# Kernel tuning notes

Measured on AMD Instinct MI355X. Metric: run time of the kernel, lower is better.

The kernel has to match this reference:

```python
import jax, jax.numpy as jnp
import numpy as np

N_NODES = 100000
N_EDGES = 800000
IN_DIM = 128
HID_DIM = 128
OUT_DIM = 128


def setup_inputs() -> dict:
    key = jax.random.key(0)
    ks = jax.random.split(key, 10)
    feat1 = jax.random.normal(ks[0], (N_NODES, IN_DIM), dtype=jnp.float32)
    feat2 = jax.random.normal(ks[1], (N_NODES, IN_DIM), dtype=jnp.float32)
    # GraphConv weights (Glorot-ish scale) and biases
    W1 = jax.random.normal(ks[2], (IN_DIM, HID_DIM), dtype=jnp.float32) * (1.0 / np.sqrt(IN_DIM))
    b1 = jnp.zeros((HID_DIM,), dtype=jnp.float32)
    W2 = jax.random.normal(ks[3], (HID_DIM, OUT_DIM), dtype=jnp.float32) * (1.0 / np.sqrt(HID_DIM))
    b2 = jnp.zeros((OUT_DIM,), dtype=jnp.float32)
    src1 = jax.random.randint(ks[4], (N_EDGES,), 0, N_NODES, dtype=jnp.int32)
    dst1 = jax.random.randint(ks[5], (N_EDGES,), 0, N_NODES, dtype=jnp.int32)
    src2 = jax.random.randint(ks[6], (N_EDGES,), 0, N_NODES, dtype=jnp.int32)
    dst2 = jax.random.randint(ks[7], (N_EDGES,), 0, N_NODES, dtype=jnp.int32)
    return {"feat1": feat1, "feat2": feat2, "W1": W1, "b1": b1, "W2": W2, "b2": b2,
            "src1": src1, "dst1": dst1, "src2": src2, "dst2": dst2}


def _graph_conv(x, src, dst, W, b, n_nodes):
    # DGL GraphConv, norm='both': h = D_in^{-1/2} A D_out^{-1/2} x W + b
    ones = jnp.ones(src.shape, dtype=x.dtype)
    deg_out = jax.ops.segment_sum(ones, src, num_segments=n_nodes)
    deg_in = jax.ops.segment_sum(ones, dst, num_segments=n_nodes)
    x = x * (jnp.maximum(deg_out, 1.0) ** -0.5)[:, None]
    x = x @ W                                 # apply linear before aggregation (equivalent math)
    agg = jax.ops.segment_sum(x[src], dst, num_segments=n_nodes)  # SpMM: gather + scatter-add
    return agg * (jnp.maximum(deg_in, 1.0) ** -0.5)[:, None] + b


def _encode(x, src, dst, Ws, bs, n_nodes):
    for i in range(len(Ws) - 1):
        x = jax.nn.relu(_graph_conv(x, src, dst, Ws[i], bs[i], n_nodes))
    return _graph_conv(x, src, dst, Ws[-1], bs[-1], n_nodes)


def reference(feat1, feat2, W1, b1, W2, b2, src1, dst1, src2, dst2):
    n = feat1.shape[0]
    Ws, bs = [W1, W2], [b1, b2]
    h1 = _encode(feat1, src1, dst1, Ws, bs, n)
    h2 = _encode(feat2, src2, dst2, Ws, bs, n)
    # per-feature z-score; torch std(0) is unbiased (ddof=1)
    z1 = (h1 - h1.mean(0)) / h1.std(0, ddof=1)
    z2 = (h2 - h2.mean(0)) / h2.std(0, ddof=1)
    return (z1, z2)
```

## Files before the change

### kernel.cpp

```cpp
#include <hip/hip_runtime.h>
#include <cstdint>
#include <cstddef>


#define SCAN_CHUNK 1024
#define NSLICES 64
#define HWORDS 25000

typedef __attribute__((ext_vector_type(8))) short bf16x8;
typedef __attribute__((ext_vector_type(4))) float f32x4;

__device__ __forceinline__ unsigned short f2bf(float f) {
    unsigned int u = __float_as_uint(f);
    unsigned int r = (u + 0x7FFFu + ((u >> 16) & 1u)) >> 16;
    return (unsigned short)r;
}
__device__ __forceinline__ float bflo(unsigned int u) { return __uint_as_float(u << 16); }
__device__ __forceinline__ float bfhi(unsigned int u) { return __uint_as_float(u & 0xffff0000u); }

__global__ __launch_bounds__(1024) void hist_kernel(
    const int* __restrict__ src1, const int* __restrict__ dst1,
    const int* __restrict__ src2, const int* __restrict__ dst2,
    unsigned int* __restrict__ part, int E)
{
    __shared__ unsigned int h[HWORDS];
    const int bid = blockIdx.x;
    const int a = bid / NSLICES, s = bid % NSLICES;
    const int* idx = a == 0 ? src1 : a == 1 ? dst1 : a == 2 ? src2 : dst2;

    for (int i = threadIdx.x; i < HWORDS; i += 1024) h[i] = 0u;
    __syncthreads();

    const int lo = (int)((long long)s * E / NSLICES);
    const int hi = (int)((long long)(s + 1) * E / NSLICES);
    for (int i = lo + threadIdx.x; i < hi; i += 1024) {
        unsigned int v = (unsigned int)idx[i];
        atomicAdd(&h[v >> 2], 1u << ((v & 3u) << 3));
    }
    __syncthreads();

    unsigned int* out = part + (size_t)bid * HWORDS;
    for (int i = threadIdx.x; i < HWORDS; i += 1024) out[i] = h[i];
}

__global__ __launch_bounds__(256) void hist_reduce(
    const unsigned int* __restrict__ part, int* __restrict__ deg, int M)
{
    int i = blockIdx.x * blockDim.x + threadIdx.x;
    if (i >= 4 * HWORDS) return;
    int a = i / HWORDS, w = i % HWORDS;
    const unsigned int* p = part + (size_t)a * NSLICES * HWORDS + w;
    unsigned int accA = 0u, accB = 0u;
#pragma unroll
    for (int s = 0; s < NSLICES; ++s) {
        unsigned int v = p[(size_t)s * HWORDS];
        accA += v & 0x00FF00FFu;
        accB += (v >> 8) & 0x00FF00FFu;
    }
    int4 r = make_int4((int)(accA & 0xFFFFu), (int)(accB & 0xFFFFu),
                       (int)(accA >> 16),     (int)(accB >> 16));
    *(int4*)(deg + (size_t)a * M + 4 * w) = r;
}

__global__ void scan_block_sums(const int* __restrict__ deg, int* __restrict__ partials,
                                int M, int goff)
{
    __shared__ int sd[256];
    const int g = blockIdx.y + goff;
    const int* d = deg + (size_t)(2 * g + 1) * M;
    int base = blockIdx.x * SCAN_CHUNK + threadIdx.x * 4;
    int s = 0;
#pragma unroll
    for (int j = 0; j < 4; ++j) { int i = base + j; if (i < M) s += d[i]; }
    sd[threadIdx.x] = s;
    __syncthreads();
    for (int off = 128; off > 0; off >>= 1) {
        if (threadIdx.x < off) sd[threadIdx.x] += sd[threadIdx.x + off];
        __syncthreads();
    }
    if (threadIdx.x == 0) partials[g * 256 + blockIdx.x] = sd[0];
}

__global__ void scan_partials(const int* __restrict__ partials, int* __restrict__ blockoff,
                              int P, int goff)
{
    __shared__ int sd[256];
    const int g = blockIdx.y + goff;
    const int* pp = partials + g * 256;
    int v = threadIdx.x < P ? pp[threadIdx.x] : 0;
    sd[threadIdx.x] = v;
    __syncthreads();
    for (int off = 1; off < 256; off <<= 1) {
        int t = threadIdx.x >= off ? sd[threadIdx.x - off] : 0;
        __syncthreads();
        sd[threadIdx.x] += t;
        __syncthreads();
    }
    if (threadIdx.x < P) blockoff[g * 256 + threadIdx.x] = sd[threadIdx.x] - v;
}

__global__ void scan_write(const int* __restrict__ deg, const int* __restrict__ blockoff,
                           int* rp0, int* rp1, int* cu0, int* cu1, int M, int goff)
{
    __shared__ int sd[256];
    const int g = blockIdx.y + goff;
    const int* d = deg + (size_t)(2 * g + 1) * M;
    int* rowptr = g ? rp1 : rp0;
    int* cursor = g ? cu1 : cu0;
    int base = blockIdx.x * SCAN_CHUNK + threadIdx.x * 4;
    int d0 = 0, d1 = 0, d2 = 0, d3 = 0;
    if (base + 0 < M) d0 = d[base + 0];
    if (base + 1 < M) d1 = d[base + 1];
    if (base + 2 < M) d2 = d[base + 2];
    if (base + 3 < M) d3 = d[base + 3];
    int tot = d0 + d1 + d2 + d3;
    sd[threadIdx.x] = tot;
    __syncthreads();
    for (int off = 1; off < 256; off <<= 1) {
        int t = threadIdx.x >= off ? sd[threadIdx.x - off] : 0;
        __syncthreads();
        sd[threadIdx.x] += t;
        __syncthreads();
    }
    int texcl = sd[threadIdx.x] - tot + blockoff[g * 256 + blockIdx.x];
    int p0 = texcl + d0, p1 = p0 + d1, p2 = p1 + d2, p3 = p2 + d3;
    if (base + 0 < M) { rowptr[base + 1] = p0; cursor[base + 0] = texcl; }
    if (base + 1 < M) { rowptr[base + 2] = p1; cursor[base + 1] = p0; }
    if (base + 2 < M) { rowptr[base + 3] = p2; cursor[base + 2] = p1; }
    if (base + 3 < M) { rowptr[base + 4] = p3; cursor[base + 3] = p2; }
    if (blockIdx.x == 0 && threadIdx.x == 0) rowptr[0] = 0;
}

__global__ __launch_bounds__(256) void csr_fill(
    const int* s0, const int* s1, const int* d0, const int* d1,
    int* cu0, int* cu1, int* co0, int* co1, int E, int M, int goff)
{
    const int g = blockIdx.y + goff;
    const int* src = g ? s1 : s0;
    const int* dst = g ? d1 : d0;
    int* cursor = g ? cu1 : cu0;
    int* colidx = g ? co1 : co0;

    const int grp = blockIdx.x & 7;
    const unsigned int nlo = (unsigned int)((long long)grp * M / 8);
    const unsigned int nspan = (unsigned int)((long long)(grp + 1) * M / 8) - nlo;
    const int nb = gridDim.x >> 3;
    const int bi = blockIdx.x >> 3;
    const int stride = nb * 256;

    for (int e = bi * 256 + threadIdx.x; e < E; e += stride) {
        int d = dst[e];
        int sv = src[e];
        if ((unsigned int)(d - nlo) < nspan) {
            int pos = atomicAdd(&cursor[d], 1);
            colidx[pos] = sv;
        }
    }
}

__global__ void wswz_kernel(const float* __restrict__ Wa, const float* __restrict__ Wb,
                            unsigned short* __restrict__ Wz)
{
    int i = blockIdx.x * 256 + threadIdx.x;
    const float* W = (i < 16384) ? Wa : Wb;
    int ii = i & 16383;
    int j = ii & 7, l = (ii >> 3) & 63, s = (ii >> 9) & 3, t = ii >> 11;
    int k = s * 32 + ((l >> 4) * 8) + j;
    int n = t * 16 + (l & 15);
    Wz[i] = f2bf(W[k * 128 + n]);
}

__global__ __launch_bounds__(256) void mfma_gemm(
    const float* X0, const float* X1, const unsigned short* __restrict__ Wz,
    const int* __restrict__ deg, unsigned short* Y0, unsigned short* Y1,
    int M, int goff)
{
    __shared__ __align__(16) unsigned short Abf[64 * 136];
    const int g = blockIdx.y + goff;
    const float* X = g ? X1 : X0;
    const int* deg_out = deg + (size_t)2 * g * M;
    unsigned short* Yh = g ? Y1 : Y0;
    const int tid  = threadIdx.x;
    const int row0 = blockIdx.x * 64;

#pragma unroll
    for (int i = 0; i < 8; ++i) {
        int idx = tid + i * 256;
        int r = idx >> 5, c4 = idx & 31;
        int gr = row0 + r;
        float4 v = make_float4(0.f, 0.f, 0.f, 0.f);
        if (gr < M) {
            v = ((const float4*)X)[(size_t)gr * 32 + c4];
            float so = rsqrtf(fmaxf((float)deg_out[gr], 1.f));
            v.x *= so; v.y *= so; v.z *= so; v.w *= so;
        }
        unsigned int lo = (unsigned int)f2bf(v.x) | ((unsigned int)f2bf(v.y) << 16);
        unsigned int hi = (unsigned int)f2bf(v.z) | ((unsigned int)f2bf(v.w) << 16);
        *(uint2*)(Abf + r * 136 + c4 * 4) = make_uint2(lo, hi);
    }
    __syncthreads();

    const int w = tid >> 6, lane = tid & 63;
    const int m = lane & 15, quad = lane >> 4;

    bf16x8 a[4];
#pragma unroll
    for (int s = 0; s < 4; ++s)
        a[s] = *(const bf16x8*)(Abf + (w * 16 + m) * 136 + s * 32 + quad * 8);

#pragma unroll
    for (int t = 0; t < 8; ++t) {
        f32x4 acc = {0.f, 0.f, 0.f, 0.f};
#pragma unroll
        for (int s = 0; s < 4; ++s) {
            bf16x8 b = *(const bf16x8*)(Wz + (((t * 4 + s) * 64 + lane) << 3));
            acc = __builtin_amdgcn_mfma_f32_16x16x32_bf16(a[s], b, acc, 0, 0, 0);
        }
        int gr  = row0 + w * 16 + quad * 4;
        int col = t * 16 + m;
#pragma unroll
        for (int r = 0; r < 4; ++r) {
            if (gr + r < M) Yh[(size_t)(gr + r) * 128 + col] = f2bf(acc[r]);
        }
    }
}

__device__ __forceinline__ void xcd_tile(int nb, int xcdmap, int goff,
                                         int& g, int& tile)
{
    if (xcdmap) {
        int bid = blockIdx.x;
        int grp = bid & 7;
        g = grp >> 2;
        tile = (bid >> 3) * 4 + (grp & 3);
    } else {
        g = goff;
        tile = blockIdx.x;
    }
}

#define G16_ACC(v)                                                              \
    a0 += bflo(v.x); a1 += bfhi(v.x); a2 += bflo(v.y); a3 += bfhi(v.y);         \
    a4 += bflo(v.z); a5 += bfhi(v.z); a6 += bflo(v.w); a7 += bfhi(v.w);

#define GATHER_ROW16                                                            \
    {                                                                           \
        for (; e + 8 <= end; e += 8) {                                          \
            int c0 = colidx[e+0], c1 = colidx[e+1], c2 = colidx[e+2], c3 = colidx[e+3]; \
            int c4_ = colidx[e+4], c5 = colidx[e+5], c6 = colidx[e+6], c7 = colidx[e+7]; \
            uint4 v0 = Yv[(size_t)c0 * 16 + lane16];                            \
            uint4 v1 = Yv[(size_t)c1 * 16 + lane16];                            \
            uint4 v2 = Yv[(size_t)c2 * 16 + lane16];                            \
            uint4 v3 = Yv[(size_t)c3 * 16 + lane16];                            \
            uint4 v4 = Yv[(size_t)c4_ * 16 + lane16];                           \
            uint4 v5 = Yv[(size_t)c5 * 16 + lane16];                            \
            uint4 v6 = Yv[(size_t)c6 * 16 + lane16];                            \
            uint4 v7 = Yv[(size_t)c7 * 16 + lane16];                            \
            G16_ACC(v0) G16_ACC(v1) G16_ACC(v2) G16_ACC(v3)                     \
            G16_ACC(v4) G16_ACC(v5) G16_ACC(v6) G16_ACC(v7)                     \
        }                                                                       \
        if (e + 4 <= end) {                                                     \
            int c0 = colidx[e+0], c1 = colidx[e+1], c2 = colidx[e+2], c3 = colidx[e+3]; \
            uint4 v0 = Yv[(size_t)c0 * 16 + lane16];                            \
            uint4 v1 = Yv[(size_t)c1 * 16 + lane16];                            \
            uint4 v2 = Yv[(size_t)c2 * 16 + lane16];                            \
            uint4 v3 = Yv[(size_t)c3 * 16 + lane16];                            \
            G16_ACC(v0) G16_ACC(v1) G16_ACC(v2) G16_ACC(v3)                     \
            e += 4;                                                             \
        }                                                                       \
        for (; e < end; ++e) {                                                  \
            int c = colidx[e];                                                  \
            uint4 v = Yv[(size_t)c * 16 + lane16];                              \
            G16_ACC(v)                                                          \
        }                                                                       \
    }

__global__ __launch_bounds__(256) void spmm_gemm(
    const uint4* Y0, const uint4* Y1, const int* rp0, const int* rp1,
    const int* ci0, const int* ci1, const unsigned short* __restrict__ Wz,
    const int* __restrict__ deg, const float* __restrict__ bias,
    unsigned short* O0, unsigned short* O1, int M, int nb, int xcdmap, int goff)
{
    __shared__ __align__(16) unsigned short Abf[64 * 136];
    int g, tile;
    xcd_tile(nb, xcdmap, goff, g, tile);
    if (tile >= nb) return;
    const uint4* Yv = g ? Y1 : Y0;
    const int* rowptr = g ? rp1 : rp0;
    const int* colidx = g ? ci1 : ci0;
    const int* deg_out = deg + (size_t)2 * g * M;
    const int* deg_in  = deg_out + M;
    unsigned short* Yh2 = g ? O1 : O0;

    const int tid  = threadIdx.x;
    const int row0 = tile * 64;
    const int lane16 = tid & 15;
    const int ng = tid >> 4;
    const float4 bv0 = ((const float4*)bias)[lane16 * 2];
    const float4 bv1 = ((const float4*)bias)[lane16 * 2 + 1];

#pragma unroll 1
    for (int p = 0; p < 4; ++p) {
        const int r = p * 16 + ng;
        const int node = row0 + r;
        float a0=0.f,a1=0.f,a2=0.f,a3=0.f,a4=0.f,a5=0.f,a6=0.f,a7=0.f;
        if (node < M) {
            int e = rowptr[node], end = rowptr[node + 1];
            GATHER_ROW16
            float si = rsqrtf(fmaxf((float)deg_in[node], 1.f));
            float so = rsqrtf(fmaxf((float)deg_out[node], 1.f));
            a0 = fmaxf(a0 * si + bv0.x, 0.f) * so;
            a1 = fmaxf(a1 * si + bv0.y, 0.f) * so;
            a2 = fmaxf(a2 * si + bv0.z, 0.f) * so;
            a3 = fmaxf(a3 * si + bv0.w, 0.f) * so;
            a4 = fmaxf(a4 * si + bv1.x, 0.f) * so;
            a5 = fmaxf(a5 * si + bv1.y, 0.f) * so;
            a6 = fmaxf(a6 * si + bv1.z, 0.f) * so;
            a7 = fmaxf(a7 * si + bv1.w, 0.f) * so;
        }
        uint4 wv;
        wv.x = (unsigned int)f2bf(a0) | ((unsigned int)f2bf(a1) << 16);
        wv.y = (unsigned int)f2bf(a2) | ((unsigned int)f2bf(a3) << 16);
        wv.z = (unsigned int)f2bf(a4) | ((unsigned int)f2bf(a5) << 16);
        wv.w = (unsigned int)f2bf(a6) | ((unsigned int)f2bf(a7) << 16);
        *(uint4*)(Abf + r * 136 + lane16 * 8) = wv;
    }
    __syncthreads();

    const int w = tid >> 6, lane = tid & 63;
    const int m = lane & 15, quad = lane >> 4;

    bf16x8 a[4];
#pragma unroll
    for (int s = 0; s < 4; ++s)
        a[s] = *(const bf16x8*)(Abf + (w * 16 + m) * 136 + s * 32 + quad * 8);

#pragma unroll
    for (int t = 0; t < 8; ++t) {
        f32x4 acc = {0.f, 0.f, 0.f, 0.f};
#pragma unroll
        for (int s = 0; s < 4; ++s) {
            bf16x8 b = *(const bf16x8*)(Wz + (((t * 4 + s) * 64 + lane) << 3));
            acc = __builtin_amdgcn_mfma_f32_16x16x32_bf16(a[s], b, acc, 0, 0, 0);
        }
        int gr  = row0 + w * 16 + quad * 4;
        int col = t * 16 + m;
#pragma unroll
        for (int r = 0; r < 4; ++r) {
            if (gr + r < M) Yh2[(size_t)(gr + r) * 128 + col] = f2bf(acc[r]);
        }
    }
}

__global__ __launch_bounds__(256) void spmm_stats(
    const uint4* Y0, const uint4* Y1, const int* rp0, const int* rp1,
    const int* ci0, const int* ci1, const int* __restrict__ deg,
    const float* __restrict__ bias, float* __restrict__ Z,
    double* __restrict__ gsum, double* __restrict__ gsumsq,
    int M, int nb, int xcdmap, int goff)
{
    __shared__ float lsum[16][128], lsq[16][128];
    int g, tile;
    xcd_tile(nb, xcdmap, goff, g, tile);
    if (tile >= nb) return;
    const uint4* Yv = g ? Y1 : Y0;
    const int* rowptr = g ? rp1 : rp0;
    const int* colidx = g ? ci1 : ci0;
    const int* deg_in = deg + (size_t)(2 * g + 1) * M;
    float* Zg = Z + (size_t)g * M * 128;
    double* gs = gsum + g * 128;
    double* gq = gsumsq + g * 128;

    const int tid  = threadIdx.x;
    const int row0 = tile * 64;
    const int lane16 = tid & 15;
    const int ng = tid >> 4;
    const float4 bv0 = ((const float4*)bias)[lane16 * 2];
    const float4 bv1 = ((const float4*)bias)[lane16 * 2 + 1];

    float s0=0.f,s1=0.f,s2=0.f,s3=0.f,s4=0.f,s5=0.f,s6=0.f,s7=0.f;
    float q0=0.f,q1=0.f,q2=0.f,q3=0.f,q4=0.f,q5=0.f,q6=0.f,q7=0.f;

#pragma unroll 1
    for (int p = 0; p < 4; ++p) {
        const int node = row0 + p * 16 + ng;
        if (node >= M) continue;
        float a0=0.f,a1=0.f,a2=0.f,a3=0.f,a4=0.f,a5=0.f,a6=0.f,a7=0.f;
        int e = rowptr[node], end = rowptr[node + 1];
        GATHER_ROW16
        float si = rsqrtf(fmaxf((float)deg_in[node], 1.f));
        float h0 = a0 * si + bv0.x, h1 = a1 * si + bv0.y;
        float h2 = a2 * si + bv0.z, h3 = a3 * si + bv0.w;
        float h4 = a4 * si + bv1.x, h5 = a5 * si + bv1.y;
        float h6 = a6 * si + bv1.z, h7 = a7 * si + bv1.w;
        ((float4*)Zg)[(size_t)node * 32 + lane16 * 2]     = make_float4(h0, h1, h2, h3);
        ((float4*)Zg)[(size_t)node * 32 + lane16 * 2 + 1] = make_float4(h4, h5, h6, h7);
        s0 += h0; s1 += h1; s2 += h2; s3 += h3;
        s4 += h4; s5 += h5; s6 += h6; s7 += h7;
        q0 += h0*h0; q1 += h1*h1; q2 += h2*h2; q3 += h3*h3;
        q4 += h4*h4; q5 += h5*h5; q6 += h6*h6; q7 += h7*h7;
    }

    const int cb = lane16 * 8;
    lsum[ng][cb+0]=s0; lsum[ng][cb+1]=s1; lsum[ng][cb+2]=s2; lsum[ng][cb+3]=s3;
    lsum[ng][cb+4]=s4; lsum[ng][cb+5]=s5; lsum[ng][cb+6]=s6; lsum[ng][cb+7]=s7;
    lsq[ng][cb+0]=q0; lsq[ng][cb+1]=q1; lsq[ng][cb+2]=q2; lsq[ng][cb+3]=q3;
    lsq[ng][cb+4]=q4; lsq[ng][cb+5]=q5; lsq[ng][cb+6]=q6; lsq[ng][cb+7]=q7;
    __syncthreads();

    if (tid < 128) {
        float s = 0.f;
#pragma unroll
        for (int g2 = 0; g2 < 16; ++g2) s += lsum[g2][tid];
        atomicAdd(&gs[tid], (double)s);
    } else {
        int c = tid - 128;
        float q = 0.f;
#pragma unroll
        for (int g2 = 0; g2 < 16; ++g2) q += lsq[g2][c];
        atomicAdd(&gq[c], (double)q);
    }
}

__global__ void meanstd_kernel(const double* __restrict__ gsum,
                               const double* __restrict__ gsumsq, int M,
                               float* __restrict__ mean, float* __restrict__ istd)
{
    int c = threadIdx.x;
    double mu  = gsum[c] / (double)M;
    double var = (gsumsq[c] - gsum[c] * mu) / (double)(M - 1);
    mean[c] = (float)mu;
    istd[c] = (float)(1.0 / sqrt(var));
}

__global__ __launch_bounds__(256) void normalize_kernel(
    float* __restrict__ Z, const float* __restrict__ mean,
    const float* __restrict__ istd, int n4_per_g, int n4tot)
{
    int i = blockIdx.x * blockDim.x + threadIdx.x;
    if (i >= n4tot) return;
    int gb = (i >= n4_per_g) ? 128 : 0;
    float4 v = ((float4*)Z)[i];
    int c4 = gb + ((i & 31) << 2);
    v.x = (v.x - mean[c4 + 0]) * istd[c4 + 0];
    v.y = (v.y - mean[c4 + 1]) * istd[c4 + 1];
    v.z = (v.z - mean[c4 + 2]) * istd[c4 + 2];
    v.w = (v.w - mean[c4 + 3]) * istd[c4 + 3];
    ((float4*)Z)[i] = v;
}

extern "C" void kernel_launch(void* const* d_in, const int* in_sizes, int n_in,
                              void* d_out, int out_size, void* d_ws, size_t ws_size,
                              hipStream_t stream)
{
    const float* feat1 = (const float*)d_in[0];
    const float* feat2 = (const float*)d_in[1];
    const float* W1    = (const float*)d_in[2];
    const float* b1    = (const float*)d_in[3];
    const float* W2    = (const float*)d_in[4];
    const float* b2    = (const float*)d_in[5];
    const int*   src1  = (const int*)d_in[6];
    const int*   dst1  = (const int*)d_in[7];
    const int*   src2  = (const int*)d_in[8];
    const int*   dst2  = (const int*)d_in[9];
    float* out = (float*)d_out;

    const int M = in_sizes[0] / 128;
    const int E = in_sizes[6];

    char* p0 = (char*)d_ws;
    char* p = p0;
    auto alloc = [&](size_t b) -> char* {
        char* r = p; p += (b + 255) & ~(size_t)255; return r;
    };

    double* gsum = (double*)alloc(256 * 8);
    double* gsq  = (double*)alloc(256 * 8);
    float*  mean = (float*)alloc(256 * 4);
    float*  istd = (float*)alloc(256 * 4);
    unsigned short* Wz = (unsigned short*)alloc(32768 * 2);
    int* deg = (int*)alloc((size_t)4 * M * 4);
    int* spart = (int*)alloc(512 * 4);
    int* blockoff = (int*)alloc(512 * 4);

    const size_t bytesRP = (size_t)(M + 1) * 4;
    const size_t bytesCU = (size_t)M * 4;
    const size_t bytesCI = (size_t)E * 4;
    const size_t bytesYh = (size_t)M * 128 * 2;
    const size_t bytesHP = (size_t)4 * NSLICES * HWORDS * 4;

    size_t fixed = (size_t)(p - p0);
    size_t need_merged = fixed + 2 * ((bytesRP + 255 & ~(size_t)255) +
                                      (bytesCU + 255 & ~(size_t)255) +
                                      (bytesCI + 255 & ~(size_t)255) +
                                      2 * ((bytesYh + 255 & ~(size_t)255)));
    const bool merged = ws_size >= need_merged + 4096;

    int *rpA, *rpB, *cuA, *cuB, *ciA, *ciB;
    unsigned short *YhA0, *YhA1, *YhB0, *YhB1;
    unsigned int* hpart;

    if (merged) {
        rpA = (int*)alloc(bytesRP);  rpB = (int*)alloc(bytesRP);
        cuA = (int*)alloc(bytesCU);  cuB = (int*)alloc(bytesCU);
        ciA = (int*)alloc(bytesCI);  ciB = (int*)alloc(bytesCI);
        YhA0 = (unsigned short*)alloc(bytesYh);
        YhA1 = (unsigned short*)alloc(bytesYh);
        YhB0 = (unsigned short*)alloc(bytesYh);
        YhB1 = (unsigned short*)alloc(bytesYh);
        hpart = (unsigned int*)YhA0;
    } else {
        rpA = (int*)alloc(bytesRP);  rpB = rpA;
        cuA = (int*)alloc(bytesCU);  cuB = cuA;
        ciA = (int*)alloc(bytesCI);  ciB = ciA;
        YhA0 = (unsigned short*)alloc(bytesYh);  YhA1 = YhA0;
        char* scratch = alloc(bytesHP + bytesYh);
        hpart = (unsigned int*)scratch;
        YhB0 = (unsigned short*)(scratch + bytesHP); YhB1 = YhB0;
    }

    unsigned short* Wz1 = Wz;
    unsigned short* Wz2 = Wz + 16384;

    const int BLK = 256;
    const int gemm_blocks = (M + 63) / 64;
    const int P = (M + SCAN_CHUNK - 1) / SCAN_CHUNK;
    const int NG = merged ? 2 : 1;

    hist_kernel<<<4 * NSLICES, 1024, 0, stream>>>(src1, dst1, src2, dst2, hpart, E);
    hist_reduce<<<(4 * HWORDS + BLK - 1) / BLK, BLK, 0, stream>>>(hpart, deg, M);
    wswz_kernel<<<128, BLK, 0, stream>>>(W1, W2, Wz);

    for (int g0 = 0; g0 < 2; g0 += NG) {
        dim3 gP(P, NG), gF(2048, NG), gG(gemm_blocks, NG);
        int spmm_blocks = merged ? 8 * ((2 * gemm_blocks + 7) / 8) : gemm_blocks;
        int xcdmap = merged ? 1 : 0;

        scan_block_sums<<<gP, BLK, 0, stream>>>(deg, spart, M, g0);
        scan_partials<<<dim3(1, NG), BLK, 0, stream>>>(spart, blockoff, P, g0);
        scan_write<<<gP, BLK, 0, stream>>>(deg, blockoff, rpA, rpB, cuA, cuB, M, g0);
        csr_fill<<<gF, BLK, 0, stream>>>(src1, src2, dst1, dst2, cuA, cuB, ciA, ciB, E, M, g0);

        mfma_gemm<<<gG, BLK, 0, stream>>>(feat1, feat2, Wz1, deg, YhA0, YhA1, M, g0);

        spmm_gemm<<<spmm_blocks, BLK, 0, stream>>>(
            (const uint4*)YhA0, (const uint4*)YhA1, rpA, rpB, ciA, ciB,
            Wz2, deg, b1, YhB0, YhB1, M, gemm_blocks, xcdmap, g0);

        hipMemsetAsync(gsum, 0, 2 * 256 * sizeof(double), stream);
        spmm_stats<<<spmm_blocks, BLK, 0, stream>>>(
            (const uint4*)YhB0, (const uint4*)YhB1, rpA, rpB, ciA, ciB,
            deg, b2, out, gsum, gsq, M, gemm_blocks, xcdmap, g0);

        meanstd_kernel<<<1, NG * 128, 0, stream>>>(
            gsum + g0 * 128, gsq + g0 * 128, M, mean + g0 * 128, istd + g0 * 128);
        int n4g = M * 32, n4tot = NG * n4g;
        normalize_kernel<<<(n4tot + BLK - 1) / BLK, BLK, 0, stream>>>(
            out + (size_t)g0 * M * 128, mean + g0 * 128, istd + g0 * 128, n4g, n4tot);
    }
}
```

Baseline: 531.8 us.

## Bucket SpMM gathers by source-node range and stage column indices in LDS

The SpMM gather in both the GEMM-fused and stats kernels now stages each tile's column indices in shared memory, falling back to global reads if the tile has more than ECAP edges. Edges are then processed in 8 passes, one per source-node range, so that at any moment all blocks touch a smaller slice of the feature table, which should raise L2/MALL hit rates. In exchange, every edge index is read and tested 8 times, the unrolling of the inner loop is lost (one load in flight per row instead of 8), and 32 fp32 accumulators per thread raise register pressure.

```diff
diff --git a/kernel.cpp b/kernel.cpp
--- a/kernel.cpp
+++ b/kernel.cpp
@@ -6,6 +6,8 @@
 #define SCAN_CHUNK 1024
 #define NSLICES 64
 #define HWORDS 25000
+#define NBUCK 8
+#define ECAP 2048
 
 typedef __attribute__((ext_vector_type(8))) short bf16x8;
 typedef __attribute__((ext_vector_type(4))) float f32x4;
@@ -239,39 +241,29 @@
     }
 }
 
-#define G16_ACC(v)                                                              \
-    a0 += bflo(v.x); a1 += bfhi(v.x); a2 += bflo(v.y); a3 += bfhi(v.y);         \
-    a4 += bflo(v.z); a5 += bfhi(v.z); a6 += bflo(v.w); a7 += bfhi(v.w);
-
-#define GATHER_ROW16                                                            \
+#define BUCKET_GATHER(ACC)                                                      \
     {                                                                           \
-        for (; e + 8 <= end; e += 8) {                                          \
-            int c0 = colidx[e+0], c1 = colidx[e+1], c2 = colidx[e+2], c3 = colidx[e+3]; \
-            int c4_ = colidx[e+4], c5 = colidx[e+5], c6 = colidx[e+6], c7 = colidx[e+7]; \
-            uint4 v0 = Yv[(size_t)c0 * 16 + lane16];                            \
-            uint4 v1 = Yv[(size_t)c1 * 16 + lane16];                            \
-            uint4 v2 = Yv[(size_t)c2 * 16 + lane16];                            \
-            uint4 v3 = Yv[(size_t)c3 * 16 + lane16];                            \
-            uint4 v4 = Yv[(size_t)c4_ * 16 + lane16];                           \
-            uint4 v5 = Yv[(size_t)c5 * 16 + lane16];                            \
-            uint4 v6 = Yv[(size_t)c6 * 16 + lane16];                            \
-            uint4 v7 = Yv[(size_t)c7 * 16 + lane16];                            \
-            G16_ACC(v0) G16_ACC(v1) G16_ACC(v2) G16_ACC(v3)                     \
-            G16_ACC(v4) G16_ACC(v5) G16_ACC(v6) G16_ACC(v7)                     \
-        }                                                                       \
-        if (e + 4 <= end) {                                                     \
-            int c0 = colidx[e+0], c1 = colidx[e+1], c2 = colidx[e+2], c3 = colidx[e+3]; \
-            uint4 v0 = Yv[(size_t)c0 * 16 + lane16];                            \
-            uint4 v1 = Yv[(size_t)c1 * 16 + lane16];                            \
-            uint4 v2 = Yv[(size_t)c2 * 16 + lane16];                            \
-            uint4 v3 = Yv[(size_t)c3 * 16 + lane16];                            \
-            G16_ACC(v0) G16_ACC(v1) G16_ACC(v2) G16_ACC(v3)                     \
-            e += 4;                                                             \
-        }                                                                       \
-        for (; e < end; ++e) {                                                  \
-            int c = colidx[e];                                                  \
-            uint4 v = Yv[(size_t)c * 16 + lane16];                              \
-            G16_ACC(v)                                                          \
+        for (int b = 0; b < NBUCK; ++b) {                                       \
+            const unsigned int blo = (unsigned int)((long long)b * M / NBUCK);  \
+            const unsigned int bspan =                                          \
+                (unsigned int)((long long)(b + 1) * M / NBUCK) - blo;           \
+            _Pragma("unroll")                                                   \
+            for (int p = 0; p < 4; ++p) {                                       \
+                const int rr = p * 16 + ng;                                     \
+                if (row0 + rr >= M) continue;                                   \
+                int e  = lrp[rr] - base0;                                       \
+                int e1 = lrp[rr + 1] - base0;                                   \
+                for (; e < e1; ++e) {                                           \
+                    int c = ovf ? colidx[base0 + e] : els[e];                   \
+                    if ((unsigned int)(c - blo) < bspan) {                      \
+                        uint4 v = Yv[(size_t)c * 16 + lane16];                  \
+                        ACC[p][0] += bflo(v.x); ACC[p][1] += bfhi(v.x);         \
+                        ACC[p][2] += bflo(v.y); ACC[p][3] += bfhi(v.y);         \
+                        ACC[p][4] += bflo(v.z); ACC[p][5] += bfhi(v.z);         \
+                        ACC[p][6] += bflo(v.w); ACC[p][7] += bfhi(v.w);         \
+                    }                                                           \
+                }                                                               \
+            }                                                                   \
         }                                                                       \
     }
 
@@ -282,6 +274,8 @@
     unsigned short* O0, unsigned short* O1, int M, int nb, int xcdmap, int goff)
 {
     __shared__ __align__(16) unsigned short Abf[64 * 136];
+    __shared__ int els[ECAP];
+    __shared__ int lrp[68];
     int g, tile;
     xcd_tile(nb, xcdmap, goff, g, tile);
     if (tile >= nb) return;
@@ -296,34 +290,50 @@
     const int row0 = tile * 64;
     const int lane16 = tid & 15;
     const int ng = tid >> 4;
+
+    const int nrow = (M - row0 < 64) ? (M - row0) : 64;
+    if (tid <= nrow) lrp[tid] = rowptr[row0 + tid];
+    __syncthreads();
+    const int base0 = lrp[0];
+    const int len = lrp[nrow] - base0;
+    const bool ovf = len > ECAP;
+    if (!ovf) for (int i = tid; i < len; i += 256) els[i] = colidx[base0 + i];
+    __syncthreads();
+
+    float acc[4][8];
+#pragma unroll
+    for (int p = 0; p < 4; ++p)
+#pragma unroll
+        for (int j = 0; j < 8; ++j) acc[p][j] = 0.f;
+
+    BUCKET_GATHER(acc)
+
     const float4 bv0 = ((const float4*)bias)[lane16 * 2];
     const float4 bv1 = ((const float4*)bias)[lane16 * 2 + 1];
-
-#pragma unroll 1
+#pragma unroll
     for (int p = 0; p < 4; ++p) {
-        const int r = p * 16 + ng;
-        const int node = row0 + r;
-        float a0=0.f,a1=0.f,a2=0.f,a3=0.f,a4=0.f,a5=0.f,a6=0.f,a7=0.f;
+        const int rr = p * 16 + ng;
+        const int node = row0 + rr;
+        float a0 = 0.f, a1 = 0.f, a2 = 0.f, a3 = 0.f;
+        float a4 = 0.f, a5 = 0.f, a6 = 0.f, a7 = 0.f;
         if (node < M) {
-            int e = rowptr[node], end = rowptr[node + 1];
-            GATHER_ROW16
             float si = rsqrtf(fmaxf((float)deg_in[node], 1.f));
             float so = rsqrtf(fmaxf((float)deg_out[node], 1.f));
-            a0 = fmaxf(a0 * si + bv0.x, 0.f) * so;
-            a1 = fmaxf(a1 * si + bv0.y, 0.f) * so;
-            a2 = fmaxf(a2 * si + bv0.z, 0.f) * so;
-            a3 = fmaxf(a3 * si + bv0.w, 0.f) * so;
-            a4 = fmaxf(a4 * si + bv1.x, 0.f) * so;
-            a5 = fmaxf(a5 * si + bv1.y, 0.f) * so;
-            a6 = fmaxf(a6 * si + bv1.z, 0.f) * so;
-            a7 = fmaxf(a7 * si + bv1.w, 0.f) * so;
+            a0 = fmaxf(acc[p][0] * si + bv0.x, 0.f) * so;
+            a1 = fmaxf(acc[p][1] * si + bv0.y, 0.f) * so;
+            a2 = fmaxf(acc[p][2] * si + bv0.z, 0.f) * so;
+            a3 = fmaxf(acc[p][3] * si + bv0.w, 0.f) * so;
+            a4 = fmaxf(acc[p][4] * si + bv1.x, 0.f) * so;
+            a5 = fmaxf(acc[p][5] * si + bv1.y, 0.f) * so;
+            a6 = fmaxf(acc[p][6] * si + bv1.z, 0.f) * so;
+            a7 = fmaxf(acc[p][7] * si + bv1.w, 0.f) * so;
         }
         uint4 wv;
         wv.x = (unsigned int)f2bf(a0) | ((unsigned int)f2bf(a1) << 16);
         wv.y = (unsigned int)f2bf(a2) | ((unsigned int)f2bf(a3) << 16);
         wv.z = (unsigned int)f2bf(a4) | ((unsigned int)f2bf(a5) << 16);
         wv.w = (unsigned int)f2bf(a6) | ((unsigned int)f2bf(a7) << 16);
-        *(uint4*)(Abf + r * 136 + lane16 * 8) = wv;
+        *(uint4*)(Abf + rr * 136 + lane16 * 8) = wv;
     }
     __syncthreads();
 
@@ -337,17 +347,17 @@
 
 #pragma unroll
     for (int t = 0; t < 8; ++t) {
-        f32x4 acc = {0.f, 0.f, 0.f, 0.f};
+        f32x4 acc2 = {0.f, 0.f, 0.f, 0.f};
 #pragma unroll
         for (int s = 0; s < 4; ++s) {
             bf16x8 b = *(const bf16x8*)(Wz + (((t * 4 + s) * 64 + lane) << 3));
-            acc = __builtin_amdgcn_mfma_f32_16x16x32_bf16(a[s], b, acc, 0, 0, 0);
+            acc2 = __builtin_amdgcn_mfma_f32_16x16x32_bf16(a[s], b, acc2, 0, 0, 0);
         }
         int gr  = row0 + w * 16 + quad * 4;
         int col = t * 16 + m;
 #pragma unroll
         for (int r = 0; r < 4; ++r) {
-            if (gr + r < M) Yh2[(size_t)(gr + r) * 128 + col] = f2bf(acc[r]);
+            if (gr + r < M) Yh2[(size_t)(gr + r) * 128 + col] = f2bf(acc2[r]);
         }
     }
 }
@@ -360,6 +370,8 @@
     int M, int nb, int xcdmap, int goff)
 {
     __shared__ float lsum[16][128], lsq[16][128];
+    __shared__ int els[ECAP];
+    __shared__ int lrp[68];
     int g, tile;
     xcd_tile(nb, xcdmap, goff, g, tile);
     if (tile >= nb) return;
@@ -375,24 +387,38 @@
     const int row0 = tile * 64;
     const int lane16 = tid & 15;
     const int ng = tid >> 4;
+
+    const int nrow = (M - row0 < 64) ? (M - row0) : 64;
+    if (tid <= nrow) lrp[tid] = rowptr[row0 + tid];
+    __syncthreads();
+    const int base0 = lrp[0];
+    const int len = lrp[nrow] - base0;
+    const bool ovf = len > ECAP;
+    if (!ovf) for (int i = tid; i < len; i += 256) els[i] = colidx[base0 + i];
+    __syncthreads();
+
+    float acc[4][8];
+#pragma unroll
+    for (int p = 0; p < 4; ++p)
+#pragma unroll
+        for (int j = 0; j < 8; ++j) acc[p][j] = 0.f;
+
+    BUCKET_GATHER(acc)
+
     const float4 bv0 = ((const float4*)bias)[lane16 * 2];
     const float4 bv1 = ((const float4*)bias)[lane16 * 2 + 1];
-
     float s0=0.f,s1=0.f,s2=0.f,s3=0.f,s4=0.f,s5=0.f,s6=0.f,s7=0.f;
     float q0=0.f,q1=0.f,q2=0.f,q3=0.f,q4=0.f,q5=0.f,q6=0.f,q7=0.f;
 
-#pragma unroll 1
+#pragma unroll
     for (int p = 0; p < 4; ++p) {
         const int node = row0 + p * 16 + ng;
         if (node >= M) continue;
-        float a0=0.f,a1=0.f,a2=0.f,a3=0.f,a4=0.f,a5=0.f,a6=0.f,a7=0.f;
-        int e = rowptr[node], end = rowptr[node + 1];
-        GATHER_ROW16
         float si = rsqrtf(fmaxf((float)deg_in[node], 1.f));
-        float h0 = a0 * si + bv0.x, h1 = a1 * si + bv0.y;
-        float h2 = a2 * si + bv0.z, h3 = a3 * si + bv0.w;
-        float h4 = a4 * si + bv1.x, h5 = a5 * si + bv1.y;
-        float h6 = a6 * si + bv1.z, h7 = a7 * si + bv1.w;
+        float h0 = acc[p][0] * si + bv0.x, h1 = acc[p][1] * si + bv0.y;
+        float h2 = acc[p][2] * si + bv0.z, h3 = acc[p][3] * si + bv0.w;
+        float h4 = acc[p][4] * si + bv1.x, h5 = acc[p][5] * si + bv1.y;
+        float h6 = acc[p][6] * si + bv1.z, h7 = acc[p][7] * si + bv1.w;
         ((float4*)Zg)[(size_t)node * 32 + lane16 * 2]     = make_float4(h0, h1, h2, h3);
         ((float4*)Zg)[(size_t)node * 32 + lane16 * 2 + 1] = make_float4(h4, h5, h6, h7);
         s0 += h0; s1 += h1; s2 += h2; s3 += h3;
```

Result: slower. 829.0 us (+55.9%).
